# Kernel optimization log

Hardware: AMD Instinct MI355X
Metric: run time of the kernel (lower is better)

Reference implementation:

```python
import jax, jax.numpy as jnp
import numpy as np

VOCAB = 128
SEQ = 2048
D_MODEL = VOCAB + SEQ   # 2176
D_EFF = SEQ
BATCH = 64


def setup_inputs() -> dict:
    key = jax.random.key(0)
    ks = jax.random.split(key, 10)
    def w(k, i, o):
        return (jax.random.normal(k, (i, o), dtype=jnp.float32) / np.sqrt(i)).astype(jnp.float32)
    return {
        "input": jax.random.randint(ks[0], (BATCH, SEQ), 0, VOCAB, dtype=jnp.int64),
        "emb": jax.random.normal(ks[1], (VOCAB, VOCAB), dtype=jnp.float32),
        "pos": jax.random.normal(ks[2], (SEQ, SEQ), dtype=jnp.float32),
        "WQ1": w(ks[3], D_MODEL, D_EFF),
        "WK1": w(ks[4], D_MODEL, D_EFF),
        "WV1": w(ks[5], D_MODEL, D_MODEL),
        "WQ2": w(ks[6], D_MODEL, VOCAB),
        "WK2": w(ks[7], D_MODEL, VOCAB),
        "WV2": w(ks[8], D_MODEL, VOCAB),
        "beta1": jnp.float32(1.0),
        "beta2": jnp.float32(1.0),
        "beta_out": jnp.float32(1.0),
    }


def reference(input, emb, pos, WQ1, WK1, WV1, WQ2, WK2, WV2, beta1, beta2, beta_out):
    B, S = input.shape
    V = emb.shape[0]
    D = V + S
    # token + positional features, concatenated: X is [B, S, D]
    E = emb[input]                                        # [B, S, V]
    P = jnp.broadcast_to(pos[None], (B, S, S))            # [B, S, S]
    X = jnp.concatenate([E, P], axis=-1)                  # [B, S, D]

    # stage 1: causal self-attention with learned beta scale
    Q1 = X @ WQ1                                          # [B, S, S]
    K1 = X @ WK1
    V1 = X @ WV1                                          # [B, S, D]
    scale1 = (D / S) ** 2
    S1 = beta1 * jnp.einsum('bqd,bkd->bqk', Q1, K1) * scale1
    causal = jnp.tril(jnp.ones((S, S), dtype=bool))       # True = keep
    S1 = jnp.where(causal[None], S1, -jnp.inf)
    A1 = jax.nn.softmax(S1, axis=-1)
    Y1 = jnp.einsum('bqk,bkd->bqd', A1, V1)
    Z1 = X + Y1                                           # [B, S, D]

    # stage 2: single-query (last token) cross-attention, no mask
    q2 = Z1[:, -1] @ WQ2                                  # [B, V]
    K2 = Z1 @ WK2                                         # [B, S, V]
    V2 = Z1 @ WV2                                         # [B, S, V]
    scale2 = (D / V) ** 2
    S2 = beta2 * jnp.einsum('bv,bsv->bs', q2, K2) * scale2
    A2 = jax.nn.softmax(S2, axis=-1)                      # [B, S]
    Y2 = jnp.einsum('bs,bsv->bv', A2, V2)                 # [B, V]

    logits = beta_out * (Y2 @ emb.T) * (D / V) ** 1.5     # [B, V]
    return logits
```

## Files before the change

kernel.cpp:

```cpp
#include <hip/hip_runtime.h>
#include <cmath>

#define SEQ 2048
#define NB 64
#define VOC 128
#define DM 2176
#define NEG_INF -1e30f

typedef __attribute__((ext_vector_type(8))) short short8;
typedef __attribute__((ext_vector_type(4))) float f32x4;
typedef __attribute__((ext_vector_type(4))) unsigned int uint4v;
typedef __attribute__((ext_vector_type(2))) unsigned int uint2v;

__device__ __forceinline__ void splitf(float x, unsigned short& h, unsigned short& l) {
    unsigned int u = __float_as_uint(x);
    h = (unsigned short)(u >> 16);
    float d = x - __uint_as_float(u & 0xFFFF0000u);
    l = (unsigned short)(__float_as_uint(d) >> 16);
}
__device__ __forceinline__ unsigned int bfpair(float x0, float x1, unsigned int& lopair) {
    unsigned int u0 = __float_as_uint(x0), u1 = __float_as_uint(x1);
    float d0 = x0 - __uint_as_float(u0 & 0xFFFF0000u);
    float d1 = x1 - __uint_as_float(u1 & 0xFFFF0000u);
    lopair = (__float_as_uint(d0) >> 16) | (__float_as_uint(d1) & 0xFFFF0000u);
    return (u0 >> 16) | (u1 & 0xFFFF0000u);
}

__global__ __launch_bounds__(256) void split_plain5(
    const float* __restrict__ i0, unsigned short* __restrict__ h0, unsigned short* __restrict__ l0, int n0,
    const float* __restrict__ i1, unsigned short* __restrict__ h1, unsigned short* __restrict__ l1, int n1,
    const float* __restrict__ i2, unsigned short* __restrict__ h2, unsigned short* __restrict__ l2, int n2,
    const float* __restrict__ i3, unsigned short* __restrict__ h3, unsigned short* __restrict__ l3, int n3,
    const float* __restrict__ i4, unsigned short* __restrict__ h4, unsigned short* __restrict__ l4, int n4)
{
    int i = blockIdx.x * 256 + threadIdx.x;
    const float* in; unsigned short *oh, *ol;
    if (i < n0) { in = i0; oh = h0; ol = l0; }
    else if ((i -= n0) < n1) { in = i1; oh = h1; ol = l1; }
    else if ((i -= n1) < n2) { in = i2; oh = h2; ol = l2; }
    else if ((i -= n2) < n3) { in = i3; oh = h3; ol = l3; }
    else if ((i -= n3) < n4) { in = i4; oh = h4; ol = l4; }
    else return;
    f32x4 v = *(const f32x4*)(in + (size_t)i * 4);
    unsigned int h01, h23, l01, l23;
    h01 = bfpair(v[0], v[1], l01);
    h23 = bfpair(v[2], v[3], l23);
    *(uint2v*)(oh + (size_t)i * 4) = (uint2v){h01, h23};
    *(uint2v*)(ol + (size_t)i * 4) = (uint2v){l01, l23};
}

__global__ __launch_bounds__(256) void splitT(
    const float* __restrict__ in, int ld, int row0,
    int NR, int NC,
    unsigned short* __restrict__ oh, unsigned short* __restrict__ ol)
{
    __shared__ float tile[32][33];
    const int r0 = blockIdx.x * 32, c0 = blockIdx.y * 32;
    const int t = threadIdx.x;
    const int x = t & 31, y = t >> 5;
    #pragma unroll
    for (int i = 0; i < 4; ++i) {
        int r = y + i * 8;
        tile[r][x] = in[(size_t)(row0 + r0 + r) * ld + c0 + x];
    }
    __syncthreads();
    #pragma unroll
    for (int i = 0; i < 4; ++i) {
        int c = y + i * 8;
        float v = tile[x][c];
        unsigned short h, l;
        splitf(v, h, l);
        size_t o = (size_t)(c0 + c) * NR + r0 + x;
        oh[o] = h; ol[o] = l;
    }
}

__global__ __launch_bounds__(256) void splitT3(
    const float* __restrict__ WK2, const float* __restrict__ WV2,
    const float* __restrict__ WQ2,
    unsigned short* __restrict__ oh, unsigned short* __restrict__ ol)
{
    __shared__ float tile[32][33];
    const int src = blockIdx.y >> 2, cblk = blockIdx.y & 3;
    const float* in = (src == 0) ? WK2 : (src == 1) ? WV2 : WQ2;
    const int r0 = blockIdx.x * 32, c0 = cblk * 32;
    const int t = threadIdx.x;
    const int x = t & 31, y = t >> 5;
    #pragma unroll
    for (int i = 0; i < 4; ++i) {
        int r = y + i * 8;
        tile[r][x] = in[(size_t)(r0 + r) * 128 + c0 + x];
    }
    __syncthreads();
    #pragma unroll
    for (int i = 0; i < 4; ++i) {
        int c = y + i * 8;
        float v = tile[x][c];
        unsigned short h, l;
        splitf(v, h, l);
        size_t o = (size_t)(src * 128 + c0 + c) * 2176 + r0 + x;
        oh[o] = h; ol[o] = l;
    }
}

struct GemmDesc {
    const unsigned short *Ah, *Al, *Bh, *Bl;
    float* C; unsigned short *Ch, *Cl;
    int lda, ldb, ldc, K, nx, mode, tri;
};

__global__ __launch_bounds__(256, 2) void gemm_nt_multi(GemmDesc d0, GemmDesc d1, int nblk0)
{
    __shared__ __align__(16) unsigned short sAh[128 * 64], sAl[128 * 64];
    __shared__ __align__(16) unsigned short sBh[128 * 64], sBl[128 * 64];
    GemmDesc d;
    int id = blockIdx.x;
    if (id < nblk0) d = d0; else { d = d1; id -= nblk0; }
    int bmi, bni;
    if (d.tri) {
        if (id < 136) {
            int bm_ = (int)((sqrtf(8.f * id + 1.f) - 1.f) * 0.5f);
            while ((bm_ + 1) * (bm_ + 2) / 2 <= id) ++bm_;
            while (bm_ * (bm_ + 1) / 2 > id) --bm_;
            bmi = bm_; bni = id - bm_ * (bm_ + 1) / 2;
        } else { bmi = 16; bni = id - 136; }
    } else { bmi = id / d.nx; bni = id % d.nx; }
    const int bm = bmi * 128, bn = bni * 128;
    const int t = threadIdx.x;
    const int lane = t & 63, wave = t >> 6;
    const int wr = wave >> 1, wc = wave & 1;
    const int lr = lane & 15;

    f32x4 acc[4][4];
    #pragma unroll
    for (int i = 0; i < 4; ++i)
        #pragma unroll
        for (int j = 0; j < 4; ++j) acc[i][j] = (f32x4){0.f, 0.f, 0.f, 0.f};

    for (int k0 = 0; k0 < d.K; k0 += 64) {
        __syncthreads();
        #pragma unroll
        for (int i = 0; i < 4; ++i) {
            int idx = t + i * 256;
            int r = idx >> 3, kc = (idx & 7) * 8;
            int off = (r * 128 + kc * 2) ^ ((r & 7) << 4);
            size_t ga = (size_t)(bm + r) * d.lda + k0 + kc;
            size_t gb = (size_t)(bn + r) * d.ldb + k0 + kc;
            *(short8*)((char*)sAh + off) = *(const short8*)(d.Ah + ga);
            *(short8*)((char*)sAl + off) = *(const short8*)(d.Al + ga);
            *(short8*)((char*)sBh + off) = *(const short8*)(d.Bh + gb);
            *(short8*)((char*)sBl + off) = *(const short8*)(d.Bl + gb);
        }
        __syncthreads();
        #pragma unroll
        for (int ks = 0; ks < 2; ++ks) {
            const int kby = ks * 64 + ((lane >> 4) << 4);
            short8 ah[4], al[4];
            #pragma unroll
            for (int rf = 0; rf < 4; ++rf) {
                int row = wr * 64 + rf * 16 + lr;
                int off = (row * 128 + kby) ^ ((row & 7) << 4);
                ah[rf] = *(const short8*)((const char*)sAh + off);
                al[rf] = *(const short8*)((const char*)sAl + off);
            }
            #pragma unroll
            for (int cf = 0; cf < 4; ++cf) {
                int col = wc * 64 + cf * 16 + lr;
                int off = (col * 128 + kby) ^ ((col & 7) << 4);
                short8 bh = *(const short8*)((const char*)sBh + off);
                short8 bl = *(const short8*)((const char*)sBl + off);
                #pragma unroll
                for (int rf = 0; rf < 4; ++rf) {
                    acc[rf][cf] = __builtin_amdgcn_mfma_f32_16x16x32_bf16(ah[rf], bh, acc[rf][cf], 0, 0, 0);
                    acc[rf][cf] = __builtin_amdgcn_mfma_f32_16x16x32_bf16(ah[rf], bl, acc[rf][cf], 0, 0, 0);
                    acc[rf][cf] = __builtin_amdgcn_mfma_f32_16x16x32_bf16(al[rf], bh, acc[rf][cf], 0, 0, 0);
                }
            }
        }
    }
    #pragma unroll
    for (int rf = 0; rf < 4; ++rf) {
        #pragma unroll
        for (int j = 0; j < 4; ++j) {
            int row = bm + wr * 64 + rf * 16 + ((lane >> 4) << 2) + j;
            #pragma unroll
            for (int cf = 0; cf < 4; ++cf) {
                int col = bn + wc * 64 + cf * 16 + lr;
                float v = acc[rf][cf][j];
                size_t o = (size_t)row * d.ldc + col;
                if (d.mode & 1) d.C[o] = v;
                if (d.mode & 2) { unsigned short h, l; splitf(v, h, l); d.Ch[o] = h; d.Cl[o] = l; }
            }
        }
    }
}

__device__ __forceinline__ float blk_reduce_max(float v, float* red, int t)
{
    red[t] = v; __syncthreads();
    #pragma unroll
    for (int s = 128; s >= 1; s >>= 1) {
        if (t < s) red[t] = fmaxf(red[t], red[t + s]);
        __syncthreads();
    }
    float r = red[0]; __syncthreads(); return r;
}
__device__ __forceinline__ float blk_reduce_sum(float v, float* red, int t)
{
    red[t] = v; __syncthreads();
    #pragma unroll
    for (int s = 128; s >= 1; s >>= 1) {
        if (t < s) red[t] += red[t + s];
        __syncthreads();
    }
    float r = red[0]; __syncthreads(); return r;
}

__global__ __launch_bounds__(256, 3) void attn_mfma(
    const int* __restrict__ tok,
    const float* __restrict__ G,
    const float* __restrict__ VpKVQ,
    const unsigned short* __restrict__ VpTh, const unsigned short* __restrict__ VpTl,
    const float* __restrict__ Tx, const float* __restrict__ plq,
    const float* __restrict__ beta1,
    float* __restrict__ O, float* __restrict__ q2)
{
    const int t = threadIdx.x;
    const int lane = t & 63, wave = t >> 6;
    const float c1 = beta1[0] * 1.12890625f;

    __shared__ __align__(16) unsigned short Ph[64 * 32], Pl[64 * 32];
    __shared__ float GT[64 * 128];
    __shared__ float m_s[64], l_s[64], rs_s[64];
    __shared__ int tq_s[64], tk_s[2][32];

    if (blockIdx.y >= 64) {
        const int bb = (blockIdx.y - 64) * 8 + blockIdx.x;
        float* a_s = GT;
        float* red_s = GT + 2048;
        float* w_s = GT + 2048 + 256;
        const int* tokb = tok + (size_t)bb * SEQ;
        const int tq = tokb[SEQ - 1];
        const float* Grow_q = G + (size_t)(SEQ - 1) * 2176;
        const float* Grow_t = G + (size_t)(2048 + tq) * 2176;

        float lmax = NEG_INF;
        for (int i = t; i < SEQ; i += 256) {
            int tk = tokb[i];
            float s = c1 * (Grow_t[2048 + tk] + Grow_t[i] + Grow_q[2048 + tk] + Grow_q[i]);
            a_s[i] = s;
            lmax = fmaxf(lmax, s);
        }
        float m = blk_reduce_max(lmax, red_s, t);
        float lsum = 0.f;
        for (int i = t; i < SEQ; i += 256) {
            float e = __expf(a_s[i] - m);
            a_s[i] = e;
            lsum += e;
        }
        float l = blk_reduce_sum(lsum, red_s, t);
        float inv = 1.f / l;
        if (t < VOC) w_s[t] = 0.f;
        __syncthreads();
        for (int i = t; i < SEQ; i += 256) {
            float a = a_s[i] * inv;
            a_s[i] = a;
            atomicAdd(&w_s[tokb[i]], a);
        }
        __syncthreads();
        const int v = t & 127, half = t >> 7;
        float acc = 0.f;
        for (int i = 0; i < 1024; ++i) {
            int s = half * 1024 + i;
            acc += a_s[s] * VpKVQ[(size_t)s * 384 + 256 + v];
        }
        if (half == 0) {
            for (int tt = 0; tt < VOC; ++tt)
                acc += w_s[tt] * VpKVQ[(size_t)(2048 + tt) * 384 + 256 + v];
        }
        red_s[t] = acc; __syncthreads();
        if (t < VOC)
            q2[bb * VOC + t] = red_s[t] + red_s[t + 128] + Tx[tq * 384 + 256 + t] + plq[t];
        return;
    }

    const int b = blockIdx.y;
    const int grp = blockIdx.x;

    const int qr = t >> 3;
    const int kb4 = (t & 7) * 4;
    const int lr = lane & 15;
    const int ksl = lane >> 4;
    const int kk0 = ksl * 8;
    const float* TvT = VpKVQ + (size_t)2048 * 384;

    const int qts[4] = {grp, 15 - grp, 16 + grp, 31 - grp};

    for (int pass = 0; pass < 4; ++pass) {
        const int q0 = qts[pass] * 64;

        __syncthreads();
        if (t < 64) {
            tq_s[t] = tok[(size_t)b * SEQ + q0 + t];
            m_s[t] = NEG_INF;
            l_s[t] = 0.f;
        }
        __syncthreads();
        {
            const int c4 = (t & 31) * 4;
            #pragma unroll
            for (int i = 0; i < 8; ++i) {
                int q = (t >> 5) + i * 8;
                f32x4 a = *(const f32x4*)&G[(size_t)(q0 + q) * 2176 + 2048 + c4];
                f32x4 g = *(const f32x4*)&G[(size_t)(2048 + tq_s[q]) * 2176 + 2048 + c4];
                *(f32x4*)&GT[q * 128 + c4] = a + g;
            }
        }
        if (t < 32) tk_s[0][t] = tok[(size_t)b * SEQ + t];
        f32x4 gqk_c[2], gtk_c[2];
        #pragma unroll
        for (int rr = 0; rr < 2; ++rr) {
            int q = qr + rr * 32;
            gqk_c[rr] = *(const f32x4*)&G[(size_t)(q0 + q) * 2176 + kb4];
            gtk_c[rr] = *(const f32x4*)&G[(size_t)(2048 + tq_s[q]) * 2176 + kb4];
        }

        f32x4 acc[4][4];
        #pragma unroll
        for (int i = 0; i < 4; ++i)
            #pragma unroll
            for (int j = 0; j < 4; ++j) acc[i][j] = (f32x4){0.f, 0.f, 0.f, 0.f};

        const int kend = q0 + 64;
        for (int k0 = 0; k0 < kend; k0 += 32) {
            const int cur = (k0 >> 5) & 1;
            __syncthreads();

            #pragma unroll
            for (int rr = 0; rr < 2; ++rr) {
                const int q = qr + rr * 32;
                const int qg = q0 + q;
                float s[4];
                #pragma unroll
                for (int j = 0; j < 4; ++j) {
                    int kg = k0 + kb4 + j;
                    s[j] = (kg <= qg)
                         ? c1 * (gqk_c[rr][j] + gtk_c[rr][j] + GT[q * 128 + tk_s[cur][kb4 + j]])
                         : NEG_INF;
                }
                float tmax = fmaxf(fmaxf(s[0], s[1]), fmaxf(s[2], s[3]));
                tmax = fmaxf(tmax, __shfl_xor(tmax, 1));
                tmax = fmaxf(tmax, __shfl_xor(tmax, 2));
                tmax = fmaxf(tmax, __shfl_xor(tmax, 4));
                const float m_old = m_s[q];
                const float mnew = fmaxf(m_old, tmax);
                float p0 = __expf(s[0] - mnew), p1 = __expf(s[1] - mnew);
                float p2 = __expf(s[2] - mnew), p3 = __expf(s[3] - mnew);
                float lsum = p0 + p1 + p2 + p3;
                lsum += __shfl_xor(lsum, 1);
                lsum += __shfl_xor(lsum, 2);
                lsum += __shfl_xor(lsum, 4);
                unsigned int l01, l23;
                unsigned int h01 = bfpair(p0, p1, l01);
                unsigned int h23 = bfpair(p2, p3, l23);
                int i16 = q * 4 + (((kb4 >> 3) + (q >> 1)) & 3);
                int pbyte = i16 * 16 + ((kb4 & 4) << 1);
                *(uint2v*)((char*)Ph + pbyte) = (uint2v){h01, h23};
                *(uint2v*)((char*)Pl + pbyte) = (uint2v){l01, l23};
                if ((t & 7) == 0) {
                    float rs = __expf(m_old - mnew);
                    m_s[q] = mnew;
                    l_s[q] = l_s[q] * rs + lsum;
                    rs_s[q] = rs;
                }
            }
            __syncthreads();

            const int k0n = (k0 + 32 < kend) ? k0 + 32 : k0;
            if (t < 32) tk_s[cur ^ 1][t] = tok[(size_t)b * SEQ + k0n + t];
            #pragma unroll
            for (int rr = 0; rr < 2; ++rr) {
                int q = qr + rr * 32;
                gqk_c[rr] = *(const f32x4*)&G[(size_t)(q0 + q) * 2176 + k0n + kb4];
                gtk_c[rr] = *(const f32x4*)&G[(size_t)(2048 + tq_s[q]) * 2176 + k0n + kb4];
            }

            short8 pah[4], pal[4];
            f32x4 rsv[4];
            #pragma unroll
            for (int qf = 0; qf < 4; ++qf) {
                int row = qf * 16 + lr;
                int i16 = row * 4 + ((ksl + (row >> 1)) & 3);
                pah[qf] = *(const short8*)((const char*)Ph + i16 * 16);
                pal[qf] = *(const short8*)((const char*)Pl + i16 * 16);
                rsv[qf] = *(const f32x4*)&rs_s[qf * 16 + ksl * 4];
            }
            #pragma unroll
            for (int qf = 0; qf < 4; ++qf)
                #pragma unroll
                for (int cf = 0; cf < 4; ++cf)
                    #pragma unroll
                    for (int j = 0; j < 4; ++j)
                        acc[qf][cf][j] *= rsv[qf][j];

            #pragma unroll
            for (int cf = 0; cf < 4; ++cf) {
                const int col = wave * 64 + cf * 16 + lr;
                const short8 vh = *(const short8*)(VpTh + (size_t)col * 2048 + k0 + kk0);
                const short8 vl = *(const short8*)(VpTl + (size_t)col * 2048 + k0 + kk0);
                float tv[8];
                #pragma unroll
                for (int i = 0; i < 8; ++i)
                    tv[i] = TvT[tk_s[cur][kk0 + i] * 384 + col];
                unsigned int th_[4], tl_[4];
                #pragma unroll
                for (int p = 0; p < 4; ++p) th_[p] = bfpair(tv[2 * p], tv[2 * p + 1], tl_[p]);
                union { uint4v u; short8 s; } cth, ctl;
                cth.u = (uint4v){th_[0], th_[1], th_[2], th_[3]};
                ctl.u = (uint4v){tl_[0], tl_[1], tl_[2], tl_[3]};
                #pragma unroll
                for (int qf = 0; qf < 4; ++qf) {
                    acc[qf][cf] = __builtin_amdgcn_mfma_f32_16x16x32_bf16(pah[qf], vh, acc[qf][cf], 0, 0, 0);
                    acc[qf][cf] = __builtin_amdgcn_mfma_f32_16x16x32_bf16(pah[qf], vl, acc[qf][cf], 0, 0, 0);
                    acc[qf][cf] = __builtin_amdgcn_mfma_f32_16x16x32_bf16(pal[qf], vh, acc[qf][cf], 0, 0, 0);
                    acc[qf][cf] = __builtin_amdgcn_mfma_f32_16x16x32_bf16(pah[qf], cth.s, acc[qf][cf], 0, 0, 0);
                    acc[qf][cf] = __builtin_amdgcn_mfma_f32_16x16x32_bf16(pah[qf], ctl.s, acc[qf][cf], 0, 0, 0);
                    acc[qf][cf] = __builtin_amdgcn_mfma_f32_16x16x32_bf16(pal[qf], cth.s, acc[qf][cf], 0, 0, 0);
                }
            }
        }
        __syncthreads();
        #pragma unroll
        for (int qf = 0; qf < 4; ++qf) {
            f32x4 lv = *(const f32x4*)&l_s[qf * 16 + ksl * 4];
            f32x4 inv;
            #pragma unroll
            for (int j = 0; j < 4; ++j) inv[j] = 1.0f / lv[j];
            #pragma unroll
            for (int j = 0; j < 4; ++j) {
                int row = q0 + qf * 16 + ksl * 4 + j;
                size_t base = ((size_t)b * SEQ + row) * 256 + wave * 64 + lr;
                #pragma unroll
                for (int cf = 0; cf < 4; ++cf)
                    O[base + cf * 16] = acc[qf][cf][j] * inv[j];
            }
        }
    }
}

__global__ __launch_bounds__(256) void s2_p3a(
    const int* __restrict__ tok, const float* __restrict__ q2,
    const float* __restrict__ Tx, const float* __restrict__ PxKVQ,
    const float* __restrict__ O, const float* __restrict__ beta2,
    float* __restrict__ part)
{
    const int b = blockIdx.y, c = blockIdx.x, t = threadIdx.x;
    const int s0 = c * 256;
    const float c2 = beta2[0] * 289.0f;

    __shared__ float q2s[VOC];
    __shared__ int   toks[256];
    __shared__ float es[256];
    __shared__ float red[256];

    if (t < VOC) q2s[t] = q2[b * VOC + t] * c2;
    toks[t] = tok[(size_t)b * SEQ + s0 + t];
    __syncthreads();

    const int s = s0 + t;
    const float* ok = O + ((size_t)b * SEQ + s) * 256;
    const float* xk = Tx + toks[t] * 384;
    const float* pk = PxKVQ + (size_t)s * 384;
    float dot = 0.f;
    #pragma unroll 8
    for (int v = 0; v < VOC; v += 4) {
        f32x4 a = *(const f32x4*)(ok + v);
        f32x4 x = *(const f32x4*)(xk + v);
        f32x4 p = *(const f32x4*)(pk + v);
        f32x4 q = *(const f32x4*)(q2s + v);
        dot += q[0] * (a[0] + x[0] + p[0]) + q[1] * (a[1] + x[1] + p[1])
             + q[2] * (a[2] + x[2] + p[2]) + q[3] * (a[3] + x[3] + p[3]);
    }
    float m = blk_reduce_max(dot, red, t);
    float e = __expf(dot - m);
    es[t] = e;
    float lsum = blk_reduce_sum(e, red, t);

    const int v = t & 127, half = t >> 7;
    float acc = 0.f;
    for (int i = 0; i < 128; ++i) {
        int si = half * 128 + i;
        float ee = es[si];
        acc += ee * (O[((size_t)b * SEQ + s0 + si) * 256 + 128 + v]
                   + Tx[toks[si] * 384 + 128 + v] + PxKVQ[(size_t)(s0 + si) * 384 + 128 + v]);
    }
    red[t] = acc; __syncthreads();
    float* pb = part + ((size_t)b * 8 + c) * 132;
    if (t < VOC) pb[t] = red[t] + red[t + 128];
    if (t == 128) { pb[128] = m; pb[129] = lsum; }
}

__global__ __launch_bounds__(128) void s2_p3b(
    const float* __restrict__ part, const float* __restrict__ emb,
    const float* __restrict__ beta_out, float* __restrict__ out)
{
    const int b = blockIdx.x, t = threadIdx.x;
    const float co = beta_out[0] * 70.09279563550022f;
    __shared__ float y2[VOC];
    const float* pb = part + (size_t)b * 8 * 132;
    float M = NEG_INF;
    #pragma unroll
    for (int c = 0; c < 8; ++c) M = fmaxf(M, pb[c * 132 + 128]);
    float L = 0.f, y = 0.f;
    #pragma unroll
    for (int c = 0; c < 8; ++c) {
        float sc = __expf(pb[c * 132 + 128] - M);
        L += pb[c * 132 + 129] * sc;
        y += pb[c * 132 + t] * sc;
    }
    y2[t] = y / L;
    __syncthreads();
    float g = 0.f;
    #pragma unroll 8
    for (int v = 0; v < VOC; ++v) g += y2[v] * emb[t * VOC + v];
    out[(size_t)b * VOC + t] = co * g;
}

extern "C" void kernel_launch(void* const* d_in, const int* in_sizes, int n_in,
                              void* d_out, int out_size, void* d_ws, size_t ws_size,
                              hipStream_t stream)
{
    const int* tok = (const int*)d_in[0];
    const float* emb = (const float*)d_in[1];
    const float* pos = (const float*)d_in[2];
    const float* WQ1 = (const float*)d_in[3];
    const float* WK1 = (const float*)d_in[4];
    const float* WV1 = (const float*)d_in[5];
    const float* WQ2 = (const float*)d_in[6];
    const float* WK2 = (const float*)d_in[7];
    const float* WV2 = (const float*)d_in[8];
    const float* beta1 = (const float*)d_in[9];
    const float* beta2 = (const float*)d_in[10];
    const float* beta_out = (const float*)d_in[11];
    float* out = (float*)d_out;

    if (ws_size < 178651136ull) return;

    char* wsb = (char*)d_ws;
    #define MB_(x) ((size_t)(x) * 1048576ull)
    float* O = (float*)(wsb + MB_(0));
    unsigned short* posH  = (unsigned short*)(wsb + MB_(0));
    unsigned short* posL  = (unsigned short*)(wsb + MB_(8));
    unsigned short* WQ1H  = (unsigned short*)(wsb + MB_(16));
    unsigned short* WQ1L  = (unsigned short*)(wsb + MB_(25));
    unsigned short* WK1H  = (unsigned short*)(wsb + MB_(34));
    unsigned short* WK1L  = (unsigned short*)(wsb + MB_(43));
    unsigned short* WV1H  = (unsigned short*)(wsb + MB_(52));
    unsigned short* WV1L  = (unsigned short*)(wsb + MB_(62));
    unsigned short* MwTH  = (unsigned short*)(wsb + MB_(72));
    unsigned short* MwTL  = (unsigned short*)(wsb + MB_(82));
    unsigned short* A1H   = (unsigned short*)(wsb + MB_(92));
    unsigned short* A1L   = (unsigned short*)(wsb + MB_(102));
    unsigned short* WV12TH= (unsigned short*)(wsb + MB_(112));
    unsigned short* WV12TL= (unsigned short*)(wsb + MB_(114));
    unsigned short* W2TH  = (unsigned short*)(wsb + MB_(116));
    unsigned short* W2TL  = (unsigned short*)(wsb + MB_(118));
    unsigned short* embH  = (unsigned short*)(wsb + MB_(120));
    unsigned short* embL  = (unsigned short*)(wsb + MB_(121));

    float* fp = (float*)(wsb + MB_(128));
    auto take = [&](size_t n) { float* p = fp; fp += n; return p; };
    float* G      = take((size_t)2176 * 2176);
    float* VpKVQ  = take((size_t)2176 * 384);
    float* PxKVQ  = take((size_t)2048 * 384);
    float* Tx     = take((size_t)128 * 384);
    unsigned short* VpTh = (unsigned short*)take((size_t)256 * 2048 / 2);
    unsigned short* VpTl = (unsigned short*)take((size_t)256 * 2048 / 2);
    float* q2     = take((size_t)NB * 128);
    float* part   = take((size_t)NB * 8 * 132);

    dim3 blk(256);
    unsigned short* nus = nullptr;
    float* nuf = nullptr;

    hipLaunchKernelGGL(split_plain5, dim3(17440), blk, 0, stream,
                       pos, posH, posL, 1048576,
                       WQ1, WQ1H, WQ1L, 1114112,
                       WK1, WK1H, WK1L, 1114112,
                       WV1, WV1H, WV1L, 1183744,
                       emb, embH, embL, 4096);
    hipLaunchKernelGGL(splitT3, dim3(68, 12), blk, 0, stream, WK2, WV2, WQ2, W2TH, W2TL);

    GemmDesc dMwT   {WK1H, WK1L, WQ1H, WQ1L, nuf, MwTH, MwTL, 2048, 2048, 2176, 2048, 17, 2, 0};
    GemmDesc dWV12T {W2TH, W2TL, WV1H, WV1L, nuf, WV12TH, WV12TL, 2176, 2176, 2176, 2176, 17, 2, 0};
    hipLaunchKernelGGL(gemm_nt_multi, dim3(289 + 51), blk, 0, stream, dMwT, dWV12T, 289);

    GemmDesc dA1    {posH, posL, MwTH + 128, MwTL + 128, nuf, A1H, A1L, 2048, 2176, 2176, 2048, 17, 2, 0};
    GemmDesc dA1e   {embH, embL, MwTH, MwTL, nuf, A1H + (size_t)2048 * 2176, A1L + (size_t)2048 * 2176,
                     128, 2176, 2176, 128, 17, 2, 0};
    hipLaunchKernelGGL(gemm_nt_multi, dim3(272 + 17), blk, 0, stream, dA1, dA1e, 272);

    GemmDesc dGtri  {A1H + 128, A1L + 128, posH, posL, G, nus, nus, 2176, 2048, 2176, 2048, 0, 1, 1};
    GemmDesc dGcol  {A1H, A1L, embH, embL, G + 2048, nus, nus, 2176, 128, 2176, 128, 1, 1, 0};
    hipLaunchKernelGGL(gemm_nt_multi, dim3(152 + 17), blk, 0, stream, dGtri, dGcol, 152);

    GemmDesc dVp    {posH, posL, WV12TH + 128, WV12TL + 128, VpKVQ, nus, nus, 2048, 2176, 384, 2048, 3, 1, 0};
    GemmDesc dPx    {posH, posL, W2TH + 128, W2TL + 128, PxKVQ, nus, nus, 2048, 2176, 384, 2048, 3, 1, 0};
    hipLaunchKernelGGL(gemm_nt_multi, dim3(48 + 48), blk, 0, stream, dVp, dPx, 48);

    GemmDesc dVpe   {embH, embL, WV12TH, WV12TL, VpKVQ + (size_t)2048 * 384, nus, nus, 128, 2176, 384, 128, 3, 1, 0};
    GemmDesc dTx    {embH, embL, W2TH, W2TL, Tx, nus, nus, 128, 2176, 384, 128, 3, 1, 0};
    hipLaunchKernelGGL(gemm_nt_multi, dim3(3 + 3), blk, 0, stream, dVpe, dTx, 3);

    hipLaunchKernelGGL(splitT, dim3(64, 8), blk, 0, stream, VpKVQ, 384, 0, 2048, 256, VpTh, VpTl);

    const float* plq = PxKVQ + (size_t)2047 * 384 + 256;
    hipLaunchKernelGGL(attn_mfma, dim3(8, 72), blk, 0, stream,
                       tok, G, VpKVQ, VpTh, VpTl, Tx, plq, beta1, O, q2);

    hipLaunchKernelGGL(s2_p3a, dim3(8, NB), blk, 0, stream, tok, q2, Tx, PxKVQ, O, beta2, part);
    hipLaunchKernelGGL(s2_p3b, dim3(NB), dim3(128), 0, stream, part, emb, beta_out, out);
}
```

Baseline: 1.229 ms.

## Software-pipeline score computation with MFMA accumulation using double-buffered P tiles

Double-buffers the probability tiles (Ph/Pl) and the rescale factors, and triple-buffers the token slots. The score and softmax step for key tile j+1 now runs after the MFMA accumulation of tile j. This removes one of the two block barriers per key tile and lets the score work overlap with matrix-core work. It costs extra LDS, which may reduce occupancy under the launch bound of 3 blocks per CU, and adds more complex buffer indexing.

```diff
diff --git a/kernel.cpp b/kernel.cpp
--- a/kernel.cpp
+++ b/kernel.cpp
@@ -229,10 +229,10 @@
     const int lane = t & 63, wave = t >> 6;
     const float c1 = beta1[0] * 1.12890625f;
 
-    __shared__ __align__(16) unsigned short Ph[64 * 32], Pl[64 * 32];
+    __shared__ __align__(16) unsigned short Ph[2][64 * 32], Pl[2][64 * 32];
     __shared__ float GT[64 * 128];
-    __shared__ float m_s[64], l_s[64], rs_s[64];
-    __shared__ int tq_s[64], tk_s[2][32];
+    __shared__ float m_s[64], l_s[64], rs_s[2][64];
+    __shared__ int tq_s[64], tk_s[3][32];
 
     if (blockIdx.y >= 64) {
         const int bb = (blockIdx.y - 64) * 8 + blockIdx.x;
@@ -297,7 +297,9 @@
     const int qts[4] = {grp, 15 - grp, 16 + grp, 31 - grp};
 
     for (int pass = 0; pass < 4; ++pass) {
-        const int q0 = qts[pass] * 64;
+        const int qt = qts[pass];
+        const int q0 = qt * 64;
+        const int niter = 2 * qt + 2;
 
         __syncthreads();
         if (t < 64) {
@@ -331,11 +333,14 @@
             #pragma unroll
             for (int j = 0; j < 4; ++j) acc[i][j] = (f32x4){0.f, 0.f, 0.f, 0.f};
 
-        const int kend = q0 + 64;
-        for (int k0 = 0; k0 < kend; k0 += 32) {
-            const int cur = (k0 >> 5) & 1;
-            __syncthreads();
-
+        auto SCORE = [&](int i) {
+            const int k0s = i * 32;
+            const int cs = i & 1;
+            const int sl = i % 3;
+            unsigned short* PhC = Ph[cs];
+            unsigned short* PlC = Pl[cs];
+            const int k0p = (i + 1 < niter) ? k0s + 32 : k0s;
+            if (t < 32) tk_s[(i + 1) % 3][t] = tok[(size_t)b * SEQ + k0p + t];
             #pragma unroll
             for (int rr = 0; rr < 2; ++rr) {
                 const int q = qr + rr * 32;
@@ -343,9 +348,9 @@
                 float s[4];
                 #pragma unroll
                 for (int j = 0; j < 4; ++j) {
-                    int kg = k0 + kb4 + j;
+                    int kg = k0s + kb4 + j;
                     s[j] = (kg <= qg)
-                         ? c1 * (gqk_c[rr][j] + gtk_c[rr][j] + GT[q * 128 + tk_s[cur][kb4 + j]])
+                         ? c1 * (gqk_c[rr][j] + gtk_c[rr][j] + GT[q * 128 + tk_s[sl][kb4 + j]])
                          : NEG_INF;
                 }
                 float tmax = fmaxf(fmaxf(s[0], s[1]), fmaxf(s[2], s[3]));
@@ -365,19 +370,27 @@
                 unsigned int h23 = bfpair(p2, p3, l23);
                 int i16 = q * 4 + (((kb4 >> 3) + (q >> 1)) & 3);
                 int pbyte = i16 * 16 + ((kb4 & 4) << 1);
-                *(uint2v*)((char*)Ph + pbyte) = (uint2v){h01, h23};
-                *(uint2v*)((char*)Pl + pbyte) = (uint2v){l01, l23};
+                *(uint2v*)((char*)PhC + pbyte) = (uint2v){h01, h23};
+                *(uint2v*)((char*)PlC + pbyte) = (uint2v){l01, l23};
                 if ((t & 7) == 0) {
                     float rs = __expf(m_old - mnew);
                     m_s[q] = mnew;
                     l_s[q] = l_s[q] * rs + lsum;
-                    rs_s[q] = rs;
+                    rs_s[cs][q] = rs;
                 }
             }
-            __syncthreads();
-
-            const int k0n = (k0 + 32 < kend) ? k0 + 32 : k0;
-            if (t < 32) tk_s[cur ^ 1][t] = tok[(size_t)b * SEQ + k0n + t];
+        };
+
+        __syncthreads();
+        SCORE(0);
+        __syncthreads();
+
+        for (int j = 0; j < niter; ++j) {
+            const int cur = j & 1;
+            const int sl = j % 3;
+            const int k0 = j * 32;
+
+            const int k0n = (j + 1 < niter) ? k0 + 32 : k0;
             #pragma unroll
             for (int rr = 0; rr < 2; ++rr) {
                 int q = qr + rr * 32;
@@ -385,23 +398,25 @@
                 gtk_c[rr] = *(const f32x4*)&G[(size_t)(2048 + tq_s[q]) * 2176 + k0n + kb4];
             }
 
+            const unsigned short* PhC = Ph[cur];
+            const unsigned short* PlC = Pl[cur];
             short8 pah[4], pal[4];
             f32x4 rsv[4];
             #pragma unroll
             for (int qf = 0; qf < 4; ++qf) {
                 int row = qf * 16 + lr;
                 int i16 = row * 4 + ((ksl + (row >> 1)) & 3);
-                pah[qf] = *(const short8*)((const char*)Ph + i16 * 16);
-                pal[qf] = *(const short8*)((const char*)Pl + i16 * 16);
-                rsv[qf] = *(const f32x4*)&rs_s[qf * 16 + ksl * 4];
+                pah[qf] = *(const short8*)((const char*)PhC + i16 * 16);
+                pal[qf] = *(const short8*)((const char*)PlC + i16 * 16);
+                rsv[qf] = *(const f32x4*)&rs_s[cur][qf * 16 + ksl * 4];
             }
             #pragma unroll
             for (int qf = 0; qf < 4; ++qf)
                 #pragma unroll
                 for (int cf = 0; cf < 4; ++cf)
                     #pragma unroll
-                    for (int j = 0; j < 4; ++j)
-                        acc[qf][cf][j] *= rsv[qf][j];
+                    for (int j2 = 0; j2 < 4; ++j2)
+                        acc[qf][cf][j2] *= rsv[qf][j2];
 
             #pragma unroll
             for (int cf = 0; cf < 4; ++cf) {
@@ -411,7 +426,7 @@
                 float tv[8];
                 #pragma unroll
                 for (int i = 0; i < 8; ++i)
-                    tv[i] = TvT[tk_s[cur][kk0 + i] * 384 + col];
+                    tv[i] = TvT[tk_s[sl][kk0 + i] * 384 + col];
                 unsigned int th_[4], tl_[4];
                 #pragma unroll
                 for (int p = 0; p < 4; ++p) th_[p] = bfpair(tv[2 * p], tv[2 * p + 1], tl_[p]);
@@ -428,8 +443,11 @@
                     acc[qf][cf] = __builtin_amdgcn_mfma_f32_16x16x32_bf16(pal[qf], cth.s, acc[qf][cf], 0, 0, 0);
                 }
             }
-        }
-        __syncthreads();
+
+            if (j + 1 < niter) SCORE(j + 1);
+            __syncthreads();
+        }
+
         #pragma unroll
         for (int qf = 0; qf < 4; ++qf) {
             f32x4 lv = *(const f32x4*)&l_s[qf * 16 + ksl * 4];
```

Result: faster. 1.174 ms, median of 2 (-4.4%).
